# Optimization experiments

Measured on AMD Instinct MI355X. Metric: run time of the kernel, lower is better.

Reference implementation:

```python
import jax, jax.numpy as jnp
import numpy as np
from math import sqrt

I = 1024  # input_size
H = 1024  # hidden_size
B = 4096  # batch


def setup_inputs() -> dict:
    key = jax.random.key(0)
    ks = jax.random.split(key, 12)
    a = 1.0 / sqrt(H)
    u = lambda k, shape: jax.random.uniform(k, shape, jnp.float32, -a, a)
    return {
        "x": jax.random.normal(ks[0], (B, I), jnp.float32),
        "hx": jax.random.normal(ks[1], (B, H), jnp.float32),
        "cx": jax.random.normal(ks[2], (B, H), jnp.float32),
        "weight_ih": u(ks[3], (4 * H, I)),
        "weight_hh": u(ks[4], (4 * H, H)),
        "bias_ih": u(ks[5], (4 * H,)),
        "bias_hh": u(ks[6], (4 * H,)),
        "W_peephole_i": u(ks[7], (H, H)),
        "W_peephole_f": u(ks[8], (H, H)),
        "W_peephole_o": u(ks[9], (H, H)),
    }


def reference(x, hx, cx, weight_ih, weight_hh, bias_ih, bias_hh,
              W_peephole_i, W_peephole_f, W_peephole_o):
    # gates: [B, 4H]
    gates = x @ weight_ih.T + bias_ih + hx @ weight_hh.T + bias_hh
    ingate, forgetgate, cellgate, outgate = jnp.split(gates, 4, axis=1)
    # F.linear(cx, W * eye) == cx * diag(W)  (diagonal peephole)
    ingate = jax.nn.sigmoid(ingate + cx * jnp.diagonal(W_peephole_i))
    forgetgate = jax.nn.sigmoid(forgetgate + cx * jnp.diagonal(W_peephole_f))
    cellgate = jnp.tanh(cellgate)
    cy = forgetgate * cx + ingate * cellgate
    # NOTE: original code reuses W_peephole_f for the output gate (faithful to source)
    outgate = jax.nn.sigmoid(outgate + cy * jnp.diagonal(W_peephole_f))
    hy = outgate * jnp.tanh(cy)
    return (hy, cy)
```

## Files before the change

kernel.cpp:

```cpp
#include <hip/hip_runtime.h>
#include <hip/hip_bf16.h>
#include <cstdint>


namespace {

constexpr int H   = 1024;
constexpr int K2  = 2048;
constexpr int BSZ = 4096;
constexpr size_t OUT_CY = (size_t)BSZ * H;

typedef __attribute__((ext_vector_type(8))) short bf16x8;
typedef __attribute__((ext_vector_type(4))) float f32x4;

__device__ __forceinline__ unsigned short f2bf(float f) {
  union { float f; uint32_t u; } v; v.f = f;
  uint32_t u = v.u;
  u += 0x7FFFu + ((u >> 16) & 1u);
  return (unsigned short)(u >> 16);
}

__device__ __forceinline__ float sigm(float x) {
  return 1.0f / (1.0f + __expf(-x));
}
__device__ __forceinline__ float tanh_fast(float x) {
  return 1.0f - 2.0f / (1.0f + __expf(2.0f * x));
}

__device__ __forceinline__ void gload_lds16(const void* g, void* l) {
  __builtin_amdgcn_global_load_lds(
      (const __attribute__((address_space(1))) void*)g,
      (__attribute__((address_space(3))) void*)l, 16, 0, 0);
}

}

__global__ __launch_bounds__(256) void cast_kernel(
    const float* __restrict__ x, const float* __restrict__ hx,
    const float* __restrict__ wih, const float* __restrict__ whh,
    unsigned short* __restrict__ A, unsigned short* __restrict__ W) {
  int b = blockIdx.x;
  bool isW = b >= 8192;
  int t = (isW ? b - 8192 : b) * 256 + threadIdx.x;
  int idx = t * 4;
  int n = idx >> 11;
  int k = idx & 2047;
  const float* s0 = isW ? wih : x;
  const float* s1 = isW ? whh : hx;
  const float* src = (k < H) ? (s0 + (size_t)n * H + k)
                             : (s1 + (size_t)n * H + (k - H));
  float4 v = *(const float4*)src;
  ushort4 o;
  o.x = f2bf(v.x); o.y = f2bf(v.y); o.z = f2bf(v.z); o.w = f2bf(v.w);
  if (isW) {
    int g = n >> 10, h = n & 1023;
    int np = ((h >> 4) << 6) + (g << 4) + (h & 15);
    *(ushort4*)(W + (size_t)np * K2 + k) = o;
  } else {
    *(ushort4*)(A + idx) = o;
  }
}

__global__ __launch_bounds__(256) void lstm_fused_gemm(
    const unsigned short* __restrict__ A,
    const unsigned short* __restrict__ W,
    const float* __restrict__ cx,
    const float* __restrict__ bias_ih, const float* __restrict__ bias_hh,
    const float* __restrict__ Wpi, const float* __restrict__ Wpf,
    float* __restrict__ out) {
  __shared__ __align__(16) unsigned short As[128 * 64];
  __shared__ __align__(16) unsigned short Ws[128 * 64];

  const int tid  = threadIdx.x;
  const int lane = tid & 63;
  const int wave = tid >> 6;
  const int wm = wave & 1;
  const int wn = wave >> 1;
  const int m0 = blockIdx.x * 128;
  const int h0 = blockIdx.y * 32;
  const int w0 = blockIdx.y * 128;

  const int srow = tid >> 3;
  const int scol = (((tid & 7) ^ (srow & 7)) << 3);

  f32x4 acc[4][4];
#pragma unroll
  for (int i = 0; i < 4; ++i)
#pragma unroll
    for (int j = 0; j < 4; ++j)
      acc[i][j] = (f32x4){0.f, 0.f, 0.f, 0.f};

  const int col  = lane & 15;
  const int quad = lane >> 4;
  const int kq   = quad * 8;

  for (int kt = 0; kt < K2 / 64; ++kt) {
    const int kb = kt * 64;
    __syncthreads();
#pragma unroll
    for (int q = 0; q < 4; ++q) {
      const int row = q * 32 + srow;
      const int ldsoff = q * 2048 + wave * 512;
      gload_lds16(A + (size_t)(m0 + row) * K2 + kb + scol, &As[ldsoff]);
      gload_lds16(W + (size_t)(w0 + row) * K2 + kb + scol, &Ws[ldsoff]);
    }
    __syncthreads();

#pragma unroll
    for (int ks = 0; ks < 2; ++ks) {
      const int kk = ks * 32 + kq;
      bf16x8 a[4], b[4];
#pragma unroll
      for (int i = 0; i < 4; ++i) {
        const int R = wm * 64 + i * 16 + col;
        a[i] = *(const bf16x8*)&As[R * 64 + ((((kk >> 3) ^ (R & 7)) << 3))];
      }
#pragma unroll
      for (int j = 0; j < 4; ++j) {
        const int R = wn * 64 + j * 16 + col;
        b[j] = *(const bf16x8*)&Ws[R * 64 + ((((kk >> 3) ^ (R & 7)) << 3))];
      }
#pragma unroll
      for (int i = 0; i < 4; ++i)
#pragma unroll
        for (int j = 0; j < 4; ++j)
          acc[i][j] = __builtin_amdgcn_mfma_f32_16x16x32_bf16(a[i], b[j], acc[i][j], 0, 0, 0);
    }
  }

  const int h = h0 + wn * 16 + col;
  const float bi = bias_ih[h]         + bias_hh[h];
  const float bf = bias_ih[H + h]     + bias_hh[H + h];
  const float bc = bias_ih[2 * H + h] + bias_hh[2 * H + h];
  const float bo = bias_ih[3 * H + h] + bias_hh[3 * H + h];
  const float di = Wpi[(size_t)h * (H + 1)];
  const float df = Wpf[(size_t)h * (H + 1)];
#pragma unroll
  for (int i = 0; i < 4; ++i) {
#pragma unroll
    for (int r = 0; r < 4; ++r) {
      const int m = m0 + wm * 64 + i * 16 + quad * 4 + r;
      const float c  = cx[(size_t)m * H + h];
      const float ip = acc[i][0][r] + bi;
      const float fp = acc[i][1][r] + bf;
      const float cp = acc[i][2][r] + bc;
      const float op = acc[i][3][r] + bo;
      const float ig = sigm(ip + c * di);
      const float fg = sigm(fp + c * df);
      const float cg = tanh_fast(cp);
      const float cy = fg * c + ig * cg;
      const float og = sigm(op + cy * df);
      const float hy = og * tanh_fast(cy);
      out[(size_t)m * H + h] = hy;
      out[OUT_CY + (size_t)m * H + h] = cy;
    }
  }
}

extern "C" void kernel_launch(void* const* d_in, const int* in_sizes, int n_in,
                              void* d_out, int out_size, void* d_ws, size_t ws_size,
                              hipStream_t stream) {
  const float* x   = (const float*)d_in[0];
  const float* hx  = (const float*)d_in[1];
  const float* cx  = (const float*)d_in[2];
  const float* wih = (const float*)d_in[3];
  const float* whh = (const float*)d_in[4];
  const float* bih = (const float*)d_in[5];
  const float* bhh = (const float*)d_in[6];
  const float* wpi = (const float*)d_in[7];
  const float* wpf = (const float*)d_in[8];
  float* out = (float*)d_out;

  unsigned short* Abf = (unsigned short*)d_ws;
  unsigned short* Wbf = Abf + (size_t)BSZ * K2;

  cast_kernel<<<16384, 256, 0, stream>>>(x, hx, wih, whh, Abf, Wbf);

  dim3 grid(BSZ / 128, H / 32);
  lstm_fused_gemm<<<grid, 256, 0, stream>>>(Abf, Wbf, cx, bih, bhh, wpi, wpf, out);
}
```

Before: 228.2 us.

## Use two waves per block with 64x128 per-wave tiles and regrouped weights

Cuts the GEMM block from four waves to two. Each wave now computes a 64x128 output tile (4x8 MFMA accumulators) instead of 64x64, so every A fragment read from LDS is reused across twice as many MFMAs. The weight interleave is changed from 16-row to 32-row gate groups so each wave's 128 columns still hold all four gates for 32 hidden units. The epilogue loops over two 16-wide hidden halves. In exchange, per-wave register use doubles (which could spill or limit occupancy, hence launch_bounds(128,2)), and each thread issues twice as many global-to-LDS loads per k-step.

```diff
diff --git a/kernel.cpp b/kernel.cpp
--- a/kernel.cpp
+++ b/kernel.cpp
@@ -54,14 +54,14 @@
   o.x = f2bf(v.x); o.y = f2bf(v.y); o.z = f2bf(v.z); o.w = f2bf(v.w);
   if (isW) {
     int g = n >> 10, h = n & 1023;
-    int np = ((h >> 4) << 6) + (g << 4) + (h & 15);
+    int np = ((h >> 5) << 7) + (g << 5) + (h & 31);
     *(ushort4*)(W + (size_t)np * K2 + k) = o;
   } else {
     *(ushort4*)(A + idx) = o;
   }
 }
 
-__global__ __launch_bounds__(256) void lstm_fused_gemm(
+__global__ __launch_bounds__(128, 2) void lstm_fused_gemm(
     const unsigned short* __restrict__ A,
     const unsigned short* __restrict__ W,
     const float* __restrict__ cx,
@@ -74,8 +74,6 @@
   const int tid  = threadIdx.x;
   const int lane = tid & 63;
   const int wave = tid >> 6;
-  const int wm = wave & 1;
-  const int wn = wave >> 1;
   const int m0 = blockIdx.x * 128;
   const int h0 = blockIdx.y * 32;
   const int w0 = blockIdx.y * 128;
@@ -83,11 +81,11 @@
   const int srow = tid >> 3;
   const int scol = (((tid & 7) ^ (srow & 7)) << 3);
 
-  f32x4 acc[4][4];
+  f32x4 acc[4][8];
 #pragma unroll
   for (int i = 0; i < 4; ++i)
 #pragma unroll
-    for (int j = 0; j < 4; ++j)
+    for (int j = 0; j < 8; ++j)
       acc[i][j] = (f32x4){0.f, 0.f, 0.f, 0.f};
 
   const int col  = lane & 15;
@@ -98,9 +96,9 @@
     const int kb = kt * 64;
     __syncthreads();
 #pragma unroll
-    for (int q = 0; q < 4; ++q) {
-      const int row = q * 32 + srow;
-      const int ldsoff = q * 2048 + wave * 512;
+    for (int p = 0; p < 8; ++p) {
+      const int row = p * 16 + srow;
+      const int ldsoff = p * 1024 + wave * 512;
       gload_lds16(A + (size_t)(m0 + row) * K2 + kb + scol, &As[ldsoff]);
       gload_lds16(W + (size_t)(w0 + row) * K2 + kb + scol, &Ws[ldsoff]);
     }
@@ -109,50 +107,53 @@
 #pragma unroll
     for (int ks = 0; ks < 2; ++ks) {
       const int kk = ks * 32 + kq;
-      bf16x8 a[4], b[4];
+      bf16x8 a[4], b[8];
 #pragma unroll
       for (int i = 0; i < 4; ++i) {
-        const int R = wm * 64 + i * 16 + col;
-        a[i] = *(const bf16x8*)&As[R * 64 + ((((kk >> 3) ^ (R & 7)) << 3))];
+        const int R = wave * 64 + i * 16 + col;
+        a[i] = *(const bf16x8*)&As[R * 64 + (((kk >> 3) ^ (R & 7)) << 3)];
       }
 #pragma unroll
-      for (int j = 0; j < 4; ++j) {
-        const int R = wn * 64 + j * 16 + col;
-        b[j] = *(const bf16x8*)&Ws[R * 64 + ((((kk >> 3) ^ (R & 7)) << 3))];
+      for (int j = 0; j < 8; ++j) {
+        const int R = j * 16 + col;
+        b[j] = *(const bf16x8*)&Ws[R * 64 + (((kk >> 3) ^ (R & 7)) << 3)];
       }
 #pragma unroll
       for (int i = 0; i < 4; ++i)
 #pragma unroll
-        for (int j = 0; j < 4; ++j)
+        for (int j = 0; j < 8; ++j)
           acc[i][j] = __builtin_amdgcn_mfma_f32_16x16x32_bf16(a[i], b[j], acc[i][j], 0, 0, 0);
     }
   }
 
-  const int h = h0 + wn * 16 + col;
-  const float bi = bias_ih[h]         + bias_hh[h];
-  const float bf = bias_ih[H + h]     + bias_hh[H + h];
-  const float bc = bias_ih[2 * H + h] + bias_hh[2 * H + h];
-  const float bo = bias_ih[3 * H + h] + bias_hh[3 * H + h];
-  const float di = Wpi[(size_t)h * (H + 1)];
-  const float df = Wpf[(size_t)h * (H + 1)];
 #pragma unroll
-  for (int i = 0; i < 4; ++i) {
+  for (int hh = 0; hh < 2; ++hh) {
+    const int h = h0 + hh * 16 + col;
+    const float bi = bias_ih[h]         + bias_hh[h];
+    const float bf = bias_ih[H + h]     + bias_hh[H + h];
+    const float bc = bias_ih[2 * H + h] + bias_hh[2 * H + h];
+    const float bo = bias_ih[3 * H + h] + bias_hh[3 * H + h];
+    const float di = Wpi[(size_t)h * (H + 1)];
+    const float df = Wpf[(size_t)h * (H + 1)];
 #pragma unroll
-    for (int r = 0; r < 4; ++r) {
-      const int m = m0 + wm * 64 + i * 16 + quad * 4 + r;
-      const float c  = cx[(size_t)m * H + h];
-      const float ip = acc[i][0][r] + bi;
-      const float fp = acc[i][1][r] + bf;
-      const float cp = acc[i][2][r] + bc;
-      const float op = acc[i][3][r] + bo;
-      const float ig = sigm(ip + c * di);
-      const float fg = sigm(fp + c * df);
-      const float cg = tanh_fast(cp);
-      const float cy = fg * c + ig * cg;
-      const float og = sigm(op + cy * df);
-      const float hy = og * tanh_fast(cy);
-      out[(size_t)m * H + h] = hy;
-      out[OUT_CY + (size_t)m * H + h] = cy;
+    for (int i = 0; i < 4; ++i) {
+#pragma unroll
+      for (int r = 0; r < 4; ++r) {
+        const int m = m0 + wave * 64 + i * 16 + quad * 4 + r;
+        const float c  = cx[(size_t)m * H + h];
+        const float ip = acc[i][0 + hh][r] + bi;
+        const float fp = acc[i][2 + hh][r] + bf;
+        const float cp = acc[i][4 + hh][r] + bc;
+        const float op = acc[i][6 + hh][r] + bo;
+        const float ig = sigm(ip + c * di);
+        const float fg = sigm(fp + c * df);
+        const float cg = tanh_fast(cp);
+        const float cy = fg * c + ig * cg;
+        const float og = sigm(op + cy * df);
+        const float hy = og * tanh_fast(cy);
+        out[(size_t)m * H + h] = hy;
+        out[OUT_CY + (size_t)m * H + h] = cy;
+      }
     }
   }
 }
@@ -177,5 +178,5 @@
   cast_kernel<<<16384, 256, 0, stream>>>(x, hx, wih, whh, Abf, Wbf);
 
   dim3 grid(BSZ / 128, H / 32);
-  lstm_fused_gemm<<<grid, 256, 0, stream>>>(Abf, Wbf, cx, bih, bhh, wpi, wpf, out);
+  lstm_fused_gemm<<<grid, 128, 0, stream>>>(Abf, Wbf, cx, bih, bhh, wpi, wpf, out);
 }
```

New measurement: 222.9 us. 2.3% less time.

## Switch to 32x32x16 MFMA with 2-wave blocks and XCD-aware tile swizzle

Applied to the files above, without the earlier changes.

Replaces the 16x16x32 MFMA tiling with 32x32x16 MFMA. Each of the two waves now computes a 64x128 tile, and the weight rows are regrouped in 32-row gate interleaving to match the new output layout. Block indices are remapped so that blocks sharing the same weight columns land on the same XCD, which is meant to improve L2 reuse. Halving the threads per block doubles the loads each thread issues. The larger accumulator raises register pressure, which is capped by launch_bounds(128,2).

```diff
diff --git a/kernel.cpp b/kernel.cpp
--- a/kernel.cpp
+++ b/kernel.cpp
@@ -8,10 +8,12 @@
 constexpr int H   = 1024;
 constexpr int K2  = 2048;
 constexpr int BSZ = 4096;
+constexpr int BK  = 64;
+constexpr int NKT = K2 / BK;
 constexpr size_t OUT_CY = (size_t)BSZ * H;
 
 typedef __attribute__((ext_vector_type(8))) short bf16x8;
-typedef __attribute__((ext_vector_type(4))) float f32x4;
+typedef __attribute__((ext_vector_type(16))) float f32x16;
 
 __device__ __forceinline__ unsigned short f2bf(float f) {
   union { float f; uint32_t u; } v; v.f = f;
@@ -54,81 +56,81 @@
   o.x = f2bf(v.x); o.y = f2bf(v.y); o.z = f2bf(v.z); o.w = f2bf(v.w);
   if (isW) {
     int g = n >> 10, h = n & 1023;
-    int np = ((h >> 4) << 6) + (g << 4) + (h & 15);
+    int np = ((h >> 5) << 7) + (g << 5) + (h & 31);
     *(ushort4*)(W + (size_t)np * K2 + k) = o;
   } else {
     *(ushort4*)(A + idx) = o;
   }
 }
 
-__global__ __launch_bounds__(256) void lstm_fused_gemm(
+__global__ __launch_bounds__(128, 2) void lstm_fused_gemm(
     const unsigned short* __restrict__ A,
     const unsigned short* __restrict__ W,
     const float* __restrict__ cx,
     const float* __restrict__ bias_ih, const float* __restrict__ bias_hh,
     const float* __restrict__ Wpi, const float* __restrict__ Wpf,
     float* __restrict__ out) {
-  __shared__ __align__(16) unsigned short As[128 * 64];
-  __shared__ __align__(16) unsigned short Ws[128 * 64];
+  __shared__ __align__(16) unsigned short As[128 * BK];
+  __shared__ __align__(16) unsigned short Ws[128 * BK];
 
   const int tid  = threadIdx.x;
   const int lane = tid & 63;
   const int wave = tid >> 6;
-  const int wm = wave & 1;
-  const int wn = wave >> 1;
-  const int m0 = blockIdx.x * 128;
-  const int h0 = blockIdx.y * 32;
-  const int w0 = blockIdx.y * 128;
 
-  const int srow = tid >> 3;
-  const int scol = (((tid & 7) ^ (srow & 7)) << 3);
+  const int flat = blockIdx.x + 32 * blockIdx.y;
+  const int xcd  = flat & 7;
+  const int slot = flat >> 3;
+  const int bx   = slot & 31;
+  const int by   = xcd * 4 + (slot >> 5);
+  const int m0 = bx * 128;
+  const int h0 = by * 32;
+  const int w0 = by * 128;
 
-  f32x4 acc[4][4];
+  const int srow  = tid >> 3;
+  const int cg8   = (((tid & 7) ^ ((tid >> 3) & 7)) << 3);
+
+  const int col32 = lane & 31;
+  const int half  = lane >> 5;
+  const int xm    = col32 & 7;
+
+  f32x16 acc[2][4];
 #pragma unroll
-  for (int i = 0; i < 4; ++i)
+  for (int i = 0; i < 2; ++i)
 #pragma unroll
     for (int j = 0; j < 4; ++j)
-      acc[i][j] = (f32x4){0.f, 0.f, 0.f, 0.f};
+      acc[i][j] = (f32x16)(0.0f);
 
-  const int col  = lane & 15;
-  const int quad = lane >> 4;
-  const int kq   = quad * 8;
-
-  for (int kt = 0; kt < K2 / 64; ++kt) {
-    const int kb = kt * 64;
+  for (int kt = 0; kt < NKT; ++kt) {
+    const int kb = kt * BK;
     __syncthreads();
 #pragma unroll
-    for (int q = 0; q < 4; ++q) {
-      const int row = q * 32 + srow;
-      const int ldsoff = q * 2048 + wave * 512;
-      gload_lds16(A + (size_t)(m0 + row) * K2 + kb + scol, &As[ldsoff]);
-      gload_lds16(W + (size_t)(w0 + row) * K2 + kb + scol, &Ws[ldsoff]);
+    for (int p = 0; p < 8; ++p) {
+      const int row = p * 16 + srow;
+      const int ldsoff = p * 1024 + tid * 8;
+      gload_lds16(A + (size_t)(m0 + row) * K2 + kb + cg8, &As[ldsoff]);
+      gload_lds16(W + (size_t)(w0 + row) * K2 + kb + cg8, &Ws[ldsoff]);
     }
     __syncthreads();
 
 #pragma unroll
-    for (int ks = 0; ks < 2; ++ks) {
-      const int kk = ks * 32 + kq;
-      bf16x8 a[4], b[4];
+    for (int s = 0; s < 4; ++s) {
+      const int cl8 = (((s * 2 + half) ^ xm) << 3);
+      bf16x8 a[2], b[4];
 #pragma unroll
-      for (int i = 0; i < 4; ++i) {
-        const int R = wm * 64 + i * 16 + col;
-        a[i] = *(const bf16x8*)&As[R * 64 + ((((kk >> 3) ^ (R & 7)) << 3))];
-      }
+      for (int i = 0; i < 2; ++i)
+        a[i] = *(const bf16x8*)&As[(wave * 64 + i * 32 + col32) * BK + cl8];
 #pragma unroll
-      for (int j = 0; j < 4; ++j) {
-        const int R = wn * 64 + j * 16 + col;
-        b[j] = *(const bf16x8*)&Ws[R * 64 + ((((kk >> 3) ^ (R & 7)) << 3))];
-      }
+      for (int j = 0; j < 4; ++j)
+        b[j] = *(const bf16x8*)&Ws[(j * 32 + col32) * BK + cl8];
 #pragma unroll
-      for (int i = 0; i < 4; ++i)
+      for (int i = 0; i < 2; ++i)
 #pragma unroll
         for (int j = 0; j < 4; ++j)
-          acc[i][j] = __builtin_amdgcn_mfma_f32_16x16x32_bf16(a[i], b[j], acc[i][j], 0, 0, 0);
+          acc[i][j] = __builtin_amdgcn_mfma_f32_32x32x16_bf16(a[i], b[j], acc[i][j], 0, 0, 0);
     }
   }
 
-  const int h = h0 + wn * 16 + col;
+  const int h = h0 + col32;
   const float bi = bias_ih[h]         + bias_hh[h];
   const float bf = bias_ih[H + h]     + bias_hh[H + h];
   const float bc = bias_ih[2 * H + h] + bias_hh[2 * H + h];
@@ -136,10 +138,10 @@
   const float di = Wpi[(size_t)h * (H + 1)];
   const float df = Wpf[(size_t)h * (H + 1)];
 #pragma unroll
-  for (int i = 0; i < 4; ++i) {
+  for (int i = 0; i < 2; ++i) {
 #pragma unroll
-    for (int r = 0; r < 4; ++r) {
-      const int m = m0 + wm * 64 + i * 16 + quad * 4 + r;
+    for (int r = 0; r < 16; ++r) {
+      const int m = m0 + wave * 64 + i * 32 + (r & 3) + 8 * (r >> 2) + 4 * half;
       const float c  = cx[(size_t)m * H + h];
       const float ip = acc[i][0][r] + bi;
       const float fp = acc[i][1][r] + bf;
@@ -177,5 +179,5 @@
   cast_kernel<<<16384, 256, 0, stream>>>(x, hx, wih, whh, Abf, Wbf);
 
   dim3 grid(BSZ / 128, H / 32);
-  lstm_fused_gemm<<<grid, 256, 0, stream>>>(Abf, Wbf, cx, bih, bhh, wpi, wpf, out);
+  lstm_fused_gemm<<<grid, 128, 0, stream>>>(Abf, Wbf, cx, bih, bhh, wpi, wpf, out);
 }
```

After: 227.4 us. No clear change (-0.4%).
